# Optimization experiments

Measured on AMD Instinct MI355X. Metric: run time of the kernel, lower is better.

Reference implementation:

```python
import jax, jax.numpy as jnp
import numpy as np

DIM = 256; HEADS = 8; WS = 7; SHIFT = 3; HID = 1024
HD = DIM // HEADS
SCALE = HD ** -0.5
EPS = 1e-5


def layer_norm(x, g, b):
    m = x.mean(-1, keepdims=True)
    v = ((x - m) ** 2).mean(-1, keepdims=True)
    return (x - m) / jnp.sqrt(v + EPS) * g + b


def window_partition(x, ws):
    B, H, W, C = x.shape
    x = x.reshape(B, H // ws, ws, W // ws, ws, C).transpose(0, 1, 3, 2, 4, 5)
    return x.reshape(-1, ws * ws, C)


def window_reverse(w, ws, H, W):
    B = w.shape[0] // ((H // ws) * (W // ws))
    x = w.reshape(B, H // ws, W // ws, ws, ws, -1).transpose(0, 1, 3, 2, 4, 5)
    return x.reshape(B, H, W, -1)


def setup_inputs() -> dict:
    key = jax.random.key(0)
    ks = jax.random.split(key, 16)
    B, H, W, C = 4, 112, 112, DIM
    L = H * W; N = WS * WS; nW = (H // WS) * (W // WS)
    def p(k, shape, s=0.02):
        return jax.random.normal(k, shape, jnp.float32) * s
    return dict(
        x=jax.random.normal(ks[0], (B, L, C), jnp.float32),
        mask_matrix=jax.random.normal(ks[1], (nW, N, N), jnp.float32),
        polar_embed=jax.random.normal(ks[2], (B, L, 2), jnp.float32),
        vote_embed=jax.random.normal(ks[3], (B, L, 3), jnp.float32),
        g1=jnp.ones((C,), jnp.float32), be1=jnp.zeros((C,), jnp.float32),
        w_qkv=p(ks[4], (3 * C, C)), b_qkv=jnp.zeros((3 * C,), jnp.float32),
        w_proj=p(ks[5], (C, C)), b_proj=jnp.zeros((C,), jnp.float32),
        tau=jnp.ones((1, HEADS, 1, 1), jnp.float32),
        rpe_w1=p(ks[6], (16, 2)), rpe_b1=jnp.zeros((16,), jnp.float32),
        rpe_w2=p(ks[7], (HEADS, 16)), rpe_b2=jnp.zeros((HEADS,), jnp.float32),
        vote_w1=p(ks[8], (16, 3)), vote_b1=jnp.zeros((16,), jnp.float32),
        vote_w2=p(ks[9], (C, 16)), vote_b2=jnp.zeros((C,), jnp.float32),
        g2=jnp.ones((C,), jnp.float32), be2=jnp.zeros((C,), jnp.float32),
        fc1_w=p(ks[10], (HID, C)), fc1_b=jnp.zeros((HID,), jnp.float32),
        fc2_w=p(ks[11], (C, HID)), fc2_b=jnp.zeros((C,), jnp.float32),
        H=H, W=W)


def reference(x, mask_matrix, polar_embed, vote_embed, g1, be1, w_qkv, b_qkv,
              w_proj, b_proj, tau, rpe_w1, rpe_b1, rpe_w2, rpe_b2,
              vote_w1, vote_b1, vote_w2, vote_b2, g2, be2,
              fc1_w, fc1_b, fc2_w, fc2_b, H, W):
    B, L, C = x.shape
    shortcut = x
    xn = layer_norm(x, g1, be1).reshape(B, H, W, C)
    pe = polar_embed.reshape(B, H, W, -1)
    ve = vote_embed.reshape(B, H, W, -1)
    pad_b = (-H) % WS; pad_r = (-W) % WS
    if pad_b or pad_r:
        xn = jnp.pad(xn, ((0, 0), (0, pad_b), (0, pad_r), (0, 0)))
        pe = jnp.pad(pe, ((0, 0), (0, pad_b), (0, pad_r), (0, 0)))
        ve = jnp.pad(ve, ((0, 0), (0, pad_b), (0, pad_r), (0, 0)))
    Hp, Wp = H + pad_b, W + pad_r
    if SHIFT > 0:
        xn = jnp.roll(xn, (-SHIFT, -SHIFT), axis=(1, 2))
        pe = jnp.roll(pe, (-SHIFT, -SHIFT), axis=(1, 2))
        ve = jnp.roll(ve, (-SHIFT, -SHIFT), axis=(1, 2))
    xw = window_partition(xn, WS)   # [B_, N, C]
    pw = window_partition(pe, WS)   # [B_, N, 2]
    vw = window_partition(ve, WS)   # [B_, N, 3]
    B_, N, _ = xw.shape
    # vote mlp: 1x1 convs == pointwise linears over channel dim
    vlin = jax.nn.relu(vw @ vote_w1.T + vote_b1) @ vote_w2.T + vote_b2  # [B_, N, DIM]
    vemb = vlin.reshape(B_, N, HEADS, HD).transpose(0, 2, 1, 3)         # [B_, h, N, d]
    qkv = (xw @ w_qkv.T + b_qkv).reshape(B_, N, 3, HEADS, HD).transpose(2, 0, 3, 1, 4)
    q = qkv[0] + vemb; k = qkv[1] + vemb; v = qkv[2] + vemb
    qn = jnp.linalg.norm(q, axis=-1, keepdims=True)
    kn = jnp.linalg.norm(k, axis=-1, keepdims=True)
    attn = jnp.einsum('bhnd,bhmd->bhnm', q, k) * SCALE
    attn = attn / jnp.maximum(qn * kn.transpose(0, 1, 3, 2), 1e-6)
    attn = attn / jnp.clip(tau, 0.01, None)
    # relative pos bias: pairwise diff of polar embed through 1x1-conv MLP
    pT = pw.transpose(0, 2, 1)                  # [B_, 2, N]
    diff = pT[:, :, :, None] - pT[:, :, None, :]  # [B_, 2, N, N]
    r = jax.nn.relu(jnp.einsum('bcnm,oc->bonm', diff, rpe_w1) + rpe_b1[None, :, None, None])
    rpe = jnp.einsum('bonm,ho->bhnm', r, rpe_w2) + rpe_b2[None, :, None, None]
    attn = attn + rpe
    if SHIFT > 0:
        nW = mask_matrix.shape[0]
        attn = attn.reshape(B_ // nW, nW, HEADS, N, N) + mask_matrix[None, :, None]
        attn = attn.reshape(B_, HEADS, N, N)
    attn = jax.nn.softmax(attn, axis=-1)
    out = jnp.einsum('bhnm,bhmd->bhnd', attn, v + vemb)
    out = out.transpose(0, 2, 1, 3).reshape(B_, N, C) @ w_proj.T + b_proj
    xr = window_reverse(out, WS, Hp, Wp)
    if SHIFT > 0:
        xr = jnp.roll(xr, (SHIFT, SHIFT), axis=(1, 2))
    xr = xr[:, :H, :W, :].reshape(B, L, C)
    x = shortcut + xr
    y = layer_norm(x, g2, be2)
    y = jax.nn.gelu(y @ fc1_w.T + fc1_b, approximate=False) @ fc2_w.T + fc2_b
    return x + y
```

## Files before the change

### kernel.cpp

```cpp
#include <hip/hip_runtime.h>
#include <hip/hip_bf16.h>
#include <math.h>

using bf16 = __hip_bfloat16;
typedef __attribute__((ext_vector_type(8))) short short8;
typedef __attribute__((ext_vector_type(4))) float f32x4;
typedef unsigned int u32;

constexpr int BB    = 4;
constexpr int Hh    = 112;
constexpr int Ww    = 112;
constexpr int C     = 256;
constexpr int L     = Hh * Ww;
constexpr int HEADS = 8;
constexpr int WS    = 7;
constexpr int SHIFT = 3;
constexpr int HID   = 1024;
constexpr int HD    = 32;
constexpr int NWIN  = 49;
constexpr int NW    = 256;
constexpr int BT    = BB * NW;
constexpr int M     = BT * NWIN;
constexpr float SCALE = 0.17677669529663687f;
constexpr float EPS   = 1e-5f;

__device__ __forceinline__ int src_row_idx(int r) {
    int b_ = r / NWIN;
    int n  = r - b_ * NWIN;
    int b  = b_ >> 8;
    int w  = b_ & 255;
    int wh = w >> 4, ww = w & 15;
    int i  = n / WS, j = n - i * WS;
    int hp = wh * WS + i, wp = ww * WS + j;
    int h  = hp + SHIFT; if (h >= Hh) h -= Hh;
    int wc = wp + SHIFT; if (wc >= Ww) wc -= Ww;
    return b * L + h * Ww + wc;
}

__device__ __forceinline__ float bf2f(short s) {
    u32 u = ((u32)(unsigned short)s) << 16;
    float f; __builtin_memcpy(&f, &u, 4); return f;
}
__device__ __forceinline__ short f2bfbits(float f) {
    bf16 b = __float2bfloat16(f);
    short s; __builtin_memcpy(&s, &b, 2); return s;
}
__device__ __forceinline__ u32 pack2bf(float lo, float hi) {
    return (u32)(unsigned short)f2bfbits(lo) | ((u32)(unsigned short)f2bfbits(hi) << 16);
}

#define GL2LDS(g, l) __builtin_amdgcn_global_load_lds( \
    (const __attribute__((address_space(1))) u32*)(const void*)(g), \
    (__attribute__((address_space(3))) u32*)(void*)(l), 16, 0, 0)

__global__ __launch_bounds__(256)
void stats_kernel(const float* __restrict__ x, float* __restrict__ stats) {
    int wave = threadIdx.x >> 6, lane = threadIdx.x & 63;
    int tok  = blockIdx.x * 4 + wave;
    const float4 v = *(const float4*)&x[(size_t)tok * C + lane * 4];
    float s  = v.x + v.y + v.z + v.w;
    float s2 = v.x*v.x + v.y*v.y + v.z*v.z + v.w*v.w;
    #pragma unroll
    for (int o = 32; o > 0; o >>= 1) {
        s  += __shfl_down(s, o);
        s2 += __shfl_down(s2, o);
    }
    if (lane == 0) {
        float m   = s * (1.0f / C);
        float var = s2 * (1.0f / C) - m * m;
        stats[tok * 2]     = m;
        stats[tok * 2 + 1] = rsqrtf(var + EPS);
    }
}

__global__ __launch_bounds__(256)
void cvt_w(const float* __restrict__ in, bf16* __restrict__ o, int n4) {
    int i = blockIdx.x * 256 + threadIdx.x;
    if (i >= n4) return;
    float4 v = *(const float4*)&in[(size_t)i * 4];
    bf16 t4[4] = {__float2bfloat16(v.x), __float2bfloat16(v.y),
                  __float2bfloat16(v.z), __float2bfloat16(v.w)};
    *(uint2*)&o[(size_t)i * 4] = *(const uint2*)t4;
}

__global__ __launch_bounds__(256)
void vemb_kernel(const float* __restrict__ vote,
                 const float* __restrict__ w1, const float* __restrict__ b1,
                 const float* __restrict__ w2, const float* __restrict__ b2,
                 bf16* __restrict__ vemb) {
    __shared__ float w2s[256][16];
    __shared__ float b2s[256];
    __shared__ float w1s[48], b1s[16];
    const int tid = threadIdx.x;
    {
        const float4* src = (const float4*)(w2 + tid * 16);
        float4* dst = (float4*)&w2s[tid][0];
        dst[0] = src[0]; dst[1] = src[1]; dst[2] = src[2]; dst[3] = src[3];
        b2s[tid] = b2[tid];
        if (tid < 48) w1s[tid] = w1[tid];
        else if (tid < 64) b1s[tid - 48] = b1[tid - 48];
    }
    __syncthreads();

    const int r = blockIdx.x * 256 + tid;
    const int srow = src_row_idx(r);
    const float v0 = vote[(size_t)srow * 3];
    const float v1 = vote[(size_t)srow * 3 + 1];
    const float v2 = vote[(size_t)srow * 3 + 2];
    float hid[16];
    #pragma unroll
    for (int o = 0; o < 16; ++o)
        hid[o] = fmaxf(fmaf(w1s[o*3], v0, fmaf(w1s[o*3+1], v1, fmaf(w1s[o*3+2], v2, b1s[o]))), 0.f);

    bf16* orow = vemb + (size_t)r * 256;
    for (int c0 = 0; c0 < 256; c0 += 8) {
        bf16 t8[8];
        #pragma unroll
        for (int j = 0; j < 8; ++j) {
            const int c = c0 + j;
            float a = b2s[c];
            #pragma unroll
            for (int o = 0; o < 16; ++o) a = fmaf(hid[o], w2s[c][o], a);
            t8[j] = __float2bfloat16(a);
        }
        *(uint4*)&orow[c0] = *(const uint4*)t8;
    }
}

enum { MODE_QKV = 0, MODE_PROJ = 1, MODE_FC1 = 2, MODE_FC2 = 3 };

template <int MODE, int NT>
__global__ __launch_bounds__(256)
void mfma_gemm(const void* __restrict__ Asrc_, const bf16* __restrict__ Wb,
               const float* __restrict__ bias, const float* __restrict__ stats,
               const float* __restrict__ gamma, const float* __restrict__ beta,
               const bf16* __restrict__ vemb, const float* __restrict__ resid,
               void* __restrict__ outp) {
    constexpr int  K  = (MODE == MODE_FC2) ? 1024 : 256;
    constexpr bool LN = (MODE == MODE_QKV) || (MODE == MODE_FC1);
    __shared__ __align__(16) char lds[32768];
    char* ldsA = lds;
    char* ldsB = lds + 16384;

    const int tid  = threadIdx.x;
    const int lane = tid & 63;
    const int wid  = tid >> 6;
    const int wr   = wid >> 1, wc = wid & 1;
    const int lrow = lane & 15, lk = lane >> 4;

    const int cpx = gridDim.x >> 3;
    const int lg  = (blockIdx.x & 7) * cpx + (blockIdx.x >> 3);
    const int bx  = lg / NT, by = lg % NT;
    const int mBase = bx * 128, nBase = by * 128;

    const int s_sub = tid >> 3;
    const int chunk = tid & 7;
    const int s_dst = (chunk * 16) ^ ((s_sub & 7) << 4);
    const char* bSrc = (const char*)(Wb + (size_t)(nBase + s_sub) * K) + s_dst;
    const char* aSrcD = (const char*)((const bf16*)Asrc_ + (size_t)(mBase + s_sub) * K) + s_dst;

    int arow[4]; float amean[4], arstd[4];
    if constexpr (LN) {
        #pragma unroll
        for (int r = 0; r < 4; ++r) {
            int row  = mBase + r * 32 + s_sub;
            int srow = (MODE == MODE_QKV) ? src_row_idx(row) : row;
            arow[r] = srow;
            amean[r] = stats[srow * 2];
            arstd[r] = stats[srow * 2 + 1];
        }
    }

    f32x4 acc[4][4] = {};

    for (int t = 0; t < K / 64; ++t) {
        const int k0 = t * 64;
        if (t) __syncthreads();
        #pragma unroll
        for (int r = 0; r < 4; ++r)
            GL2LDS(bSrc + (size_t)r * 64 * K + (size_t)t * 128,
                   ldsB + r * 4096 + wid * 1024);
        if constexpr (!LN) {
            #pragma unroll
            for (int r = 0; r < 4; ++r)
                GL2LDS(aSrcD + (size_t)r * 64 * K + (size_t)t * 128,
                       ldsA + r * 4096 + wid * 1024);
        } else {
            const int kk = k0 + chunk * 8;
            float4 g0  = *(const float4*)&gamma[kk];
            float4 g1v = *(const float4*)&gamma[kk + 4];
            float4 b0  = *(const float4*)&beta[kk];
            float4 b1v = *(const float4*)&beta[kk + 4];
            #pragma unroll
            for (int r = 0; r < 4; ++r) {
                const float* src = (const float*)Asrc_ + (size_t)arow[r] * K + kk;
                float4 v0 = *(const float4*)src;
                float4 v1 = *(const float4*)(src + 4);
                float m = amean[r], sd = arstd[r];
                bf16 tb[8];
                tb[0] = __float2bfloat16((v0.x - m) * sd * g0.x  + b0.x);
                tb[1] = __float2bfloat16((v0.y - m) * sd * g0.y  + b0.y);
                tb[2] = __float2bfloat16((v0.z - m) * sd * g0.z  + b0.z);
                tb[3] = __float2bfloat16((v0.w - m) * sd * g0.w  + b0.w);
                tb[4] = __float2bfloat16((v1.x - m) * sd * g1v.x + b1v.x);
                tb[5] = __float2bfloat16((v1.y - m) * sd * g1v.y + b1v.y);
                tb[6] = __float2bfloat16((v1.z - m) * sd * g1v.z + b1v.z);
                tb[7] = __float2bfloat16((v1.w - m) * sd * g1v.w + b1v.w);
                *(short8*)(ldsA + (r * 32 + s_sub) * 128 + s_dst) = *(const short8*)tb;
            }
        }
        __syncthreads();
        const int sw = (lrow & 7) << 4;
        #pragma unroll
        for (int ks = 0; ks < 2; ++ks) {
            const int kbl = (ks * 64 + lk * 16) ^ sw;
            short8 af[4], bfr[4];
            #pragma unroll
            for (int q = 0; q < 4; ++q) {
                af[q]  = *(const short8*)(ldsA + (wr * 64 + q * 16 + lrow) * 128 + kbl);
                bfr[q] = *(const short8*)(ldsB + (wc * 64 + q * 16 + lrow) * 128 + kbl);
            }
            #pragma unroll
            for (int mi = 0; mi < 4; ++mi)
                #pragma unroll
                for (int ni = 0; ni < 4; ++ni)
                    acc[mi][ni] = __builtin_amdgcn_mfma_f32_16x16x32_bf16(
                        af[mi], bfr[ni], acc[mi][ni], 0, 0, 0);
        }
    }

    const int cB = nBase + wc * 64 + lrow;
    const int rB = mBase + wr * 64 + lk * 4;
    float bs[4];
    #pragma unroll
    for (int ni = 0; ni < 4; ++ni) bs[ni] = bias[cB + ni * 16];
    #pragma unroll
    for (int mi = 0; mi < 4; ++mi) {
        #pragma unroll
        for (int i = 0; i < 4; ++i) {
            const int r = rB + mi * 16 + i;
            const int dst = (MODE == MODE_PROJ) ? src_row_idx(r) : r;
            #pragma unroll
            for (int ni = 0; ni < 4; ++ni) {
                const int c = cB + ni * 16;
                float v = acc[mi][ni][i] + bs[ni];
                if constexpr (MODE == MODE_QKV) {
                    float ve = __bfloat162float(vemb[(size_t)r * 256 + (c & 255)]);
                    v += (c >= 512) ? 2.f * ve : ve;
                    ((bf16*)outp)[(size_t)r * 768 + c] = __float2bfloat16(v);
                } else if constexpr (MODE == MODE_PROJ) {
                    ((float*)outp)[(size_t)dst * 256 + c] =
                        resid[(size_t)dst * 256 + c] + v;
                } else if constexpr (MODE == MODE_FC1) {
                    float gl = 0.5f * v * (1.f + erff(v * 0.70710678118f));
                    ((bf16*)outp)[(size_t)r * 1024 + c] = __float2bfloat16(gl);
                } else {
                    ((float*)outp)[(size_t)r * 256 + c] =
                        resid[(size_t)r * 256 + c] + v;
                }
            }
        }
    }
}

__global__ __launch_bounds__(256)
void attn_kernel(const bf16* __restrict__ qkv, const float* __restrict__ polar,
                 const float* __restrict__ rw1, const float* __restrict__ rb1,
                 const float* __restrict__ rw2, const float* __restrict__ rb2,
                 const float* __restrict__ tau, const float* __restrict__ mask,
                 bf16* __restrict__ outp) {
    const int w  = blockIdx.x;
    const int wl = w & 255;
    const int t  = threadIdx.x;
    const int lane = t & 63, wid = t >> 6;
    const int l15 = lane & 15, q4 = lane >> 4;
    const size_t wbase = (size_t)w * NWIN;
    const short* qs = (const short*)qkv;

    __shared__ float pwx[NWIN], pwy[NWIN];
    __shared__ float rqn[8][64], rkn[8][64];
    __shared__ float cw1s[32], cb1s[16], cw2s[8][16], rb2s[8], scts[8];
    __shared__ short rpem[8][2401];

    if (t < 98) {
        int n = t >> 1, cix = t & 1;
        int srow = src_row_idx(w * NWIN + n);
        float v = polar[(size_t)srow * 2 + cix];
        if (cix) pwy[n] = v; else pwx[n] = v;
    }
    if (t >= 128 && t < 256) {
        int u = t - 128;
        if (u < 128) cw2s[u >> 4][u & 15] = rw2[u];
    }
    if (t < 32) cw1s[t] = rw1[t];
    else if (t < 48) cb1s[t - 32] = rb1[t - 32];
    else if (t < 56) rb2s[t - 48] = rb2[t - 48];
    else if (t < 64) scts[t - 56] = SCALE / fmaxf(tau[t - 56], 0.01f);

    for (int idx = t; idx < 8 * NWIN; idx += 256) {
        int h = idx / NWIN, n = idx - h * NWIN;
        const bf16* qp = qkv + (wbase + n) * 768 + h * 32;
        float sq = 0, sk = 0;
        #pragma unroll
        for (int c = 0; c < 4; ++c) {
            short8 qv = *(const short8*)(qp + c * 8);
            short8 kv = *(const short8*)(qp + 256 + c * 8);
            #pragma unroll
            for (int j = 0; j < 8; ++j) {
                float qf = bf2f(qv[j]); sq += qf * qf;
                float kf = bf2f(kv[j]); sk += kf * kf;
            }
        }
        rqn[h][n] = rsqrtf(sq);
        rkn[h][n] = rsqrtf(sk);
    }
    __syncthreads();

    for (int e = t; e < NWIN * NWIN; e += 256) {
        int n = e / NWIN, m = e - n * NWIN;
        float dx = pwx[n] - pwx[m], dy = pwy[n] - pwy[m];
        float hid[16];
        #pragma unroll
        for (int o = 0; o < 16; ++o)
            hid[o] = fmaxf(fmaf(cw1s[2*o], dx, fmaf(cw1s[2*o+1], dy, cb1s[o])), 0.f);
        float mv = mask[(size_t)wl * NWIN * NWIN + e];
        #pragma unroll
        for (int h = 0; h < 8; ++h) {
            float a = rb2s[h] + mv;
            #pragma unroll
            for (int o = 0; o < 16; ++o) a = fmaf(hid[o], cw2s[h][o], a);
            rpem[h][e] = f2bfbits(a);
        }
    }
    __syncthreads();

    const short8 z8 = {0,0,0,0,0,0,0,0};
    const int qa  = (q4 & 1) * 2;
    const int sel = q4 >> 1;

    for (int hh = 0; hh < 2; ++hh) {
        const int h = wid + hh * 4;
        const bf16* hbase = qkv + wbase * 768 + h * 32;
        const float sct = scts[h];

        short8 kf[4], qf[4];
        #pragma unroll
        for (int at = 0; at < 4; ++at) {
            int m = at * 16 + l15;
            kf[at] = (m < NWIN) ? *(const short8*)(hbase + (size_t)m * 768 + 256 + q4 * 8) : z8;
        }
        #pragma unroll
        for (int nt = 0; nt < 4; ++nt) {
            int n = nt * 16 + l15;
            qf[nt] = (n < NWIN) ? *(const short8*)(hbase + (size_t)n * 768 + q4 * 8) : z8;
        }
        short8 vb[2][2];
        #pragma unroll
        for (int ks = 0; ks < 2; ++ks)
            #pragma unroll
            for (int ct = 0; ct < 2; ++ct) {
                short tmp[8];
                #pragma unroll
                for (int j = 0; j < 8; ++j) {
                    int m = ks * 32 + q4 * 8 + j;
                    tmp[j] = (m < NWIN)
                        ? qs[(wbase + m) * 768 + 512 + h * 32 + ct * 16 + l15]
                        : (short)0;
                }
                __builtin_memcpy(&vb[ks][ct], tmp, 16);
            }

        u32 pw[4][4][2];
        const f32x4 zf = {0.f, 0.f, 0.f, 0.f};
        #pragma unroll
        for (int nt = 0; nt < 4; ++nt) {
            f32x4 sacc[4];
            #pragma unroll
            for (int at = 0; at < 4; ++at)
                sacc[at] = __builtin_amdgcn_mfma_f32_16x16x32_bf16(kf[at], qf[nt], zf, 0, 0, 0);
            const int n = nt * 16 + l15;
            const float rq = rqn[h][n];
            float pv[4][4];
            #pragma unroll
            for (int at = 0; at < 4; ++at)
                #pragma unroll
                for (int i = 0; i < 4; ++i) {
                    int m = at * 16 + q4 * 4 + i;
                    float val = -1e30f;
                    if (n < NWIN && m < NWIN) {
                        float rr = fminf(rq * rkn[h][m], 1e6f);
                        val = sacc[at][i] * sct * rr + bf2f(rpem[h][n * NWIN + m]);
                    }
                    pv[at][i] = val;
                }
            float mx = -1e30f;
            #pragma unroll
            for (int at = 0; at < 4; ++at)
                #pragma unroll
                for (int i = 0; i < 4; ++i) mx = fmaxf(mx, pv[at][i]);
            mx = fmaxf(mx, __shfl_xor(mx, 16));
            mx = fmaxf(mx, __shfl_xor(mx, 32));
            float sum = 0.f;
            #pragma unroll
            for (int at = 0; at < 4; ++at)
                #pragma unroll
                for (int i = 0; i < 4; ++i) {
                    float ev = __expf(pv[at][i] - mx);
                    pv[at][i] = ev; sum += ev;
                }
            sum += __shfl_xor(sum, 16);
            sum += __shfl_xor(sum, 32);
            const float inv = 1.0f / sum;
            #pragma unroll
            for (int at = 0; at < 4; ++at) {
                pw[nt][at][0] = pack2bf(pv[at][0] * inv, pv[at][1] * inv);
                pw[nt][at][1] = pack2bf(pv[at][2] * inv, pv[at][3] * inv);
            }
        }

        f32x4 o[4][2] = {};
        #pragma unroll
        for (int nt = 0; nt < 4; ++nt) {
            #pragma unroll
            for (int ks = 0; ks < 2; ++ks) {
                u32 wv[4];
                #pragma unroll
                for (int w_ = 0; w_ < 4; ++w_) {
                    int srcl = l15 + (qa + (w_ >> 1)) * 16;
                    u32 lo = (u32)__shfl((int)pw[nt][2 * ks][w_ & 1], srcl);
                    u32 hi = (u32)__shfl((int)pw[nt][2 * ks + 1][w_ & 1], srcl);
                    wv[w_] = sel ? hi : lo;
                }
                short8 pa;
                __builtin_memcpy(&pa, wv, 16);
                #pragma unroll
                for (int ct = 0; ct < 2; ++ct)
                    o[nt][ct] = __builtin_amdgcn_mfma_f32_16x16x32_bf16(pa, vb[ks][ct], o[nt][ct], 0, 0, 0);
            }
        }

        #pragma unroll
        for (int nt = 0; nt < 4; ++nt)
            #pragma unroll
            for (int ct = 0; ct < 2; ++ct)
                #pragma unroll
                for (int i = 0; i < 4; ++i) {
                    int n = nt * 16 + q4 * 4 + i;
                    if (n < NWIN)
                        outp[(wbase + n) * 256 + h * 32 + ct * 16 + l15] =
                            __float2bfloat16(o[nt][ct][i]);
                }
    }
}

extern "C" void kernel_launch(void* const* d_in, const int* in_sizes, int n_in,
                              void* d_out, int out_size, void* d_ws, size_t ws_size,
                              hipStream_t stream) {
    const float* x     = (const float*)d_in[0];
    const float* mask  = (const float*)d_in[1];
    const float* polar = (const float*)d_in[2];
    const float* vote  = (const float*)d_in[3];
    const float* g1    = (const float*)d_in[4];
    const float* be1   = (const float*)d_in[5];
    const float* wqkv  = (const float*)d_in[6];
    const float* bqkv  = (const float*)d_in[7];
    const float* wproj = (const float*)d_in[8];
    const float* bproj = (const float*)d_in[9];
    const float* tau   = (const float*)d_in[10];
    const float* rw1   = (const float*)d_in[11];
    const float* rb1   = (const float*)d_in[12];
    const float* rw2   = (const float*)d_in[13];
    const float* rb2   = (const float*)d_in[14];
    const float* vw1   = (const float*)d_in[15];
    const float* vb1   = (const float*)d_in[16];
    const float* vw2   = (const float*)d_in[17];
    const float* vb2   = (const float*)d_in[18];
    const float* g2    = (const float*)d_in[19];
    const float* be2   = (const float*)d_in[20];
    const float* fc1w  = (const float*)d_in[21];
    const float* fc1b  = (const float*)d_in[22];
    const float* fc2w  = (const float*)d_in[23];
    const float* fc2b  = (const float*)d_in[24];
    float* out = (float*)d_out;

    char* base = (char*)d_ws;
    bf16*  qkv     = (bf16*)base;
    bf16*  vemb    = (bf16*)(base + 77070336);
    bf16*  attnout = (bf16*)(base + 77070336);
    bf16*  hbuf    = (bf16*)base;
    bf16*  wqkvb   = (bf16*)(base + 102760448);
    bf16*  wprojb  = wqkvb + 768 * 256;
    bf16*  fc1wb   = wprojb + 256 * 256;
    bf16*  fc2wb   = fc1wb + 1024 * 256;
    float* stats1  = (float*)(base + 104333312);
    float* stats2  = stats1 + 2 * M;

    cvt_w<<<192, 256, 0, stream>>>(wqkv, wqkvb, 768*256/4);
    cvt_w<<<64,  256, 0, stream>>>(wproj, wprojb, 256*256/4);
    cvt_w<<<256, 256, 0, stream>>>(fc1w, fc1wb, 1024*256/4);
    cvt_w<<<256, 256, 0, stream>>>(fc2w, fc2wb, 256*1024/4);

    stats_kernel<<<M / 4, 256, 0, stream>>>(x, stats1);
    vemb_kernel<<<M / 256, 256, 0, stream>>>(vote, vw1, vb1, vw2, vb2, vemb);

    mfma_gemm<MODE_QKV, 6><<<(M / 128) * 6, 256, 0, stream>>>(
        x, wqkvb, bqkv, stats1, g1, be1, vemb, nullptr, qkv);

    attn_kernel<<<BT, 256, 0, stream>>>(qkv, polar, rw1, rb1, rw2, rb2, tau, mask, attnout);

    mfma_gemm<MODE_PROJ, 2><<<(M / 128) * 2, 256, 0, stream>>>(
        attnout, wprojb, bproj, nullptr, nullptr, nullptr, nullptr, x, out);

    stats_kernel<<<M / 4, 256, 0, stream>>>(out, stats2);

    mfma_gemm<MODE_FC1, 8><<<(M / 128) * 8, 256, 0, stream>>>(
        out, fc1wb, fc1b, stats2, g2, be2, nullptr, nullptr, hbuf);

    mfma_gemm<MODE_FC2, 2><<<(M / 128) * 2, 256, 0, stream>>>(
        hbuf, fc2wb, fc2b, nullptr, nullptr, nullptr, nullptr, out, out);
}
```

Baseline: 369.6 us.

## Double-buffer LDS tiles in MFMA GEMM to overlap loads with compute

Splits the shared-memory staging buffers into two halves and prefetches the next K-tile of A and B (global-to-LDS for B and non-LN A, register staging for LayerNorm A) while MFMAs run on the current tile. This halves the barriers per iteration and is meant to hide global-memory latency behind compute. LDS use doubles to 64 KB per block, which may reduce occupancy, and register pressure rises from the staged A values.

Measured after the change: 372.3 us. About the same (+0.7%).

```diff
diff --git a/kernel.cpp b/kernel.cpp
--- a/kernel.cpp
+++ b/kernel.cpp
@@ -137,10 +137,10 @@
                const bf16* __restrict__ vemb, const float* __restrict__ resid,
                void* __restrict__ outp) {
     constexpr int  K  = (MODE == MODE_FC2) ? 1024 : 256;
+    constexpr int  T  = K / 64;
     constexpr bool LN = (MODE == MODE_QKV) || (MODE == MODE_FC1);
-    __shared__ __align__(16) char lds[32768];
-    char* ldsA = lds;
-    char* ldsB = lds + 16384;
+    __shared__ __align__(16) char ldsA[2][16384];
+    __shared__ __align__(16) char ldsB[2][16384];
 
     const int tid  = threadIdx.x;
     const int lane = tid & 63;
@@ -156,7 +156,7 @@
     const int s_sub = tid >> 3;
     const int chunk = tid & 7;
     const int s_dst = (chunk * 16) ^ ((s_sub & 7) << 4);
-    const char* bSrc = (const char*)(Wb + (size_t)(nBase + s_sub) * K) + s_dst;
+    const char* bSrc  = (const char*)(Wb + (size_t)(nBase + s_sub) * K) + s_dst;
     const char* aSrcD = (const char*)((const bf16*)Asrc_ + (size_t)(mBase + s_sub) * K) + s_dst;
 
     int arow[4]; float amean[4], arstd[4];
@@ -171,54 +171,82 @@
         }
     }
 
+    float4 sa0[4], sa1[4];
+    float4 sg0, sg1, sb0, sb1;
+
+    auto issueA = [&](int tt) {
+        const int kk = tt * 64 + chunk * 8;
+        sg0 = *(const float4*)&gamma[kk];
+        sg1 = *(const float4*)&gamma[kk + 4];
+        sb0 = *(const float4*)&beta[kk];
+        sb1 = *(const float4*)&beta[kk + 4];
+        #pragma unroll
+        for (int r = 0; r < 4; ++r) {
+            const float* src = (const float*)Asrc_ + (size_t)arow[r] * K + kk;
+            sa0[r] = *(const float4*)src;
+            sa1[r] = *(const float4*)(src + 4);
+        }
+    };
+    auto writeA = [&](int tt) {
+        char* dst = ldsA[tt & 1];
+        #pragma unroll
+        for (int r = 0; r < 4; ++r) {
+            float m = amean[r], sd = arstd[r];
+            bf16 tb[8];
+            tb[0] = __float2bfloat16((sa0[r].x - m) * sd * sg0.x + sb0.x);
+            tb[1] = __float2bfloat16((sa0[r].y - m) * sd * sg0.y + sb0.y);
+            tb[2] = __float2bfloat16((sa0[r].z - m) * sd * sg0.z + sb0.z);
+            tb[3] = __float2bfloat16((sa0[r].w - m) * sd * sg0.w + sb0.w);
+            tb[4] = __float2bfloat16((sa1[r].x - m) * sd * sg1.x + sb1.x);
+            tb[5] = __float2bfloat16((sa1[r].y - m) * sd * sg1.y + sb1.y);
+            tb[6] = __float2bfloat16((sa1[r].z - m) * sd * sg1.z + sb1.z);
+            tb[7] = __float2bfloat16((sa1[r].w - m) * sd * sg1.w + sb1.w);
+            *(short8*)(dst + (r * 32 + s_sub) * 128 + s_dst) = *(const short8*)tb;
+        }
+    };
+
     f32x4 acc[4][4] = {};
-
-    for (int t = 0; t < K / 64; ++t) {
-        const int k0 = t * 64;
-        if (t) __syncthreads();
+    const int sw = (lrow & 7) << 4;
+
+    #pragma unroll
+    for (int r = 0; r < 4; ++r)
+        GL2LDS(bSrc + (size_t)r * 64 * K, ldsB[0] + r * 4096 + wid * 1024);
+    if constexpr (!LN) {
         #pragma unroll
         for (int r = 0; r < 4; ++r)
-            GL2LDS(bSrc + (size_t)r * 64 * K + (size_t)t * 128,
-                   ldsB + r * 4096 + wid * 1024);
-        if constexpr (!LN) {
+            GL2LDS(aSrcD + (size_t)r * 64 * K, ldsA[0] + r * 4096 + wid * 1024);
+    } else {
+        issueA(0);
+        writeA(0);
+    }
+    __syncthreads();
+
+    #pragma unroll
+    for (int t = 0; t < T; ++t) {
+        if (t + 1 < T) {
             #pragma unroll
             for (int r = 0; r < 4; ++r)
-                GL2LDS(aSrcD + (size_t)r * 64 * K + (size_t)t * 128,
-                       ldsA + r * 4096 + wid * 1024);
-        } else {
-            const int kk = k0 + chunk * 8;
-            float4 g0  = *(const float4*)&gamma[kk];
-            float4 g1v = *(const float4*)&gamma[kk + 4];
-            float4 b0  = *(const float4*)&beta[kk];
-            float4 b1v = *(const float4*)&beta[kk + 4];
-            #pragma unroll
-            for (int r = 0; r < 4; ++r) {
-                const float* src = (const float*)Asrc_ + (size_t)arow[r] * K + kk;
-                float4 v0 = *(const float4*)src;
-                float4 v1 = *(const float4*)(src + 4);
-                float m = amean[r], sd = arstd[r];
-                bf16 tb[8];
-                tb[0] = __float2bfloat16((v0.x - m) * sd * g0.x  + b0.x);
-                tb[1] = __float2bfloat16((v0.y - m) * sd * g0.y  + b0.y);
-                tb[2] = __float2bfloat16((v0.z - m) * sd * g0.z  + b0.z);
-                tb[3] = __float2bfloat16((v0.w - m) * sd * g0.w  + b0.w);
-                tb[4] = __float2bfloat16((v1.x - m) * sd * g1v.x + b1v.x);
-                tb[5] = __float2bfloat16((v1.y - m) * sd * g1v.y + b1v.y);
-                tb[6] = __float2bfloat16((v1.z - m) * sd * g1v.z + b1v.z);
-                tb[7] = __float2bfloat16((v1.w - m) * sd * g1v.w + b1v.w);
-                *(short8*)(ldsA + (r * 32 + s_sub) * 128 + s_dst) = *(const short8*)tb;
-            }
-        }
-        __syncthreads();
-        const int sw = (lrow & 7) << 4;
+                GL2LDS(bSrc + (size_t)r * 64 * K + (size_t)(t + 1) * 128,
+                       ldsB[(t + 1) & 1] + r * 4096 + wid * 1024);
+            if constexpr (!LN) {
+                #pragma unroll
+                for (int r = 0; r < 4; ++r)
+                    GL2LDS(aSrcD + (size_t)r * 64 * K + (size_t)(t + 1) * 128,
+                           ldsA[(t + 1) & 1] + r * 4096 + wid * 1024);
+            } else {
+                issueA(t + 1);
+            }
+        }
+        const char* cA = ldsA[t & 1];
+        const char* cB = ldsB[t & 1];
         #pragma unroll
         for (int ks = 0; ks < 2; ++ks) {
             const int kbl = (ks * 64 + lk * 16) ^ sw;
             short8 af[4], bfr[4];
             #pragma unroll
             for (int q = 0; q < 4; ++q) {
-                af[q]  = *(const short8*)(ldsA + (wr * 64 + q * 16 + lrow) * 128 + kbl);
-                bfr[q] = *(const short8*)(ldsB + (wc * 64 + q * 16 + lrow) * 128 + kbl);
+                af[q]  = *(const short8*)(cA + (wr * 64 + q * 16 + lrow) * 128 + kbl);
+                bfr[q] = *(const short8*)(cB + (wc * 64 + q * 16 + lrow) * 128 + kbl);
             }
             #pragma unroll
             for (int mi = 0; mi < 4; ++mi)
@@ -227,13 +255,17 @@
                     acc[mi][ni] = __builtin_amdgcn_mfma_f32_16x16x32_bf16(
                         af[mi], bfr[ni], acc[mi][ni], 0, 0, 0);
         }
-    }
-
-    const int cB = nBase + wc * 64 + lrow;
-    const int rB = mBase + wr * 64 + lk * 4;
+        if (t + 1 < T) {
+            if constexpr (LN) writeA(t + 1);
+            __syncthreads();
+        }
+    }
+
+    const int cBc = nBase + wc * 64 + lrow;
+    const int rB  = mBase + wr * 64 + lk * 4;
     float bs[4];
     #pragma unroll
-    for (int ni = 0; ni < 4; ++ni) bs[ni] = bias[cB + ni * 16];
+    for (int ni = 0; ni < 4; ++ni) bs[ni] = bias[cBc + ni * 16];
     #pragma unroll
     for (int mi = 0; mi < 4; ++mi) {
         #pragma unroll
@@ -242,7 +274,7 @@
             const int dst = (MODE == MODE_PROJ) ? src_row_idx(r) : r;
             #pragma unroll
             for (int ni = 0; ni < 4; ++ni) {
-                const int c = cB + ni * 16;
+                const int c = cBc + ni * 16;
                 float v = acc[mi][ni][i] + bs[ni];
                 if constexpr (MODE == MODE_QKV) {
                     float ve = __bfloat162float(vemb[(size_t)r * 256 + (c & 255)]);
```

## Fuse FC1, GELU and FC2 into one MLP kernel keeping hidden tile in LDS

Applied to the files above, without the earlier changes.

Replaces the separate FC1 and FC2 GEMMs with a single fused kernel. Each 64-row block computes the hidden activations chunk by chunk, applies GELU, stages them in LDS as bf16, and accumulates the FC2 output, so the large hidden buffer never round-trips through global memory. A new prep kernel applies LayerNorm2 and writes a bf16 normalized input in place of the stats pass. In exchange, the 64-row tiles give less weight reuse, the activation operand is read directly from global memory, and the loop has many barriers. Occupancy may also be lower because of the larger LDS footprint.

Measured after the change: 476.4 us. 1.29x slower.

```diff
diff --git a/kernel.cpp b/kernel.cpp
--- a/kernel.cpp
+++ b/kernel.cpp
@@ -74,6 +74,29 @@
 }
 
 __global__ __launch_bounds__(256)
+void prep2_kernel(const float* __restrict__ x, const float* __restrict__ g,
+                  const float* __restrict__ b, bf16* __restrict__ o) {
+    int wave = threadIdx.x >> 6, lane = threadIdx.x & 63;
+    int tok  = blockIdx.x * 4 + wave;
+    float4 v = *(const float4*)&x[(size_t)tok * C + lane * 4];
+    float s  = v.x + v.y + v.z + v.w;
+    float s2 = v.x*v.x + v.y*v.y + v.z*v.z + v.w*v.w;
+    #pragma unroll
+    for (int ofs = 32; ofs > 0; ofs >>= 1) {
+        s  += __shfl_xor(s, ofs);
+        s2 += __shfl_xor(s2, ofs);
+    }
+    float m    = s * (1.f / C);
+    float rstd = rsqrtf(s2 * (1.f / C) - m * m + EPS);
+    float4 gv = *(const float4*)&g[lane * 4];
+    float4 bv = *(const float4*)&b[lane * 4];
+    uint2 u;
+    u.x = pack2bf((v.x - m) * rstd * gv.x + bv.x, (v.y - m) * rstd * gv.y + bv.y);
+    u.y = pack2bf((v.z - m) * rstd * gv.z + bv.z, (v.w - m) * rstd * gv.w + bv.w);
+    *(uint2*)&o[(size_t)tok * C + lane * 4] = u;
+}
+
+__global__ __launch_bounds__(256)
 void cvt_w(const float* __restrict__ in, bf16* __restrict__ o, int n4) {
     int i = blockIdx.x * 256 + threadIdx.x;
     if (i >= n4) return;
@@ -127,7 +150,7 @@
     }
 }
 
-enum { MODE_QKV = 0, MODE_PROJ = 1, MODE_FC1 = 2, MODE_FC2 = 3 };
+enum { MODE_QKV = 0, MODE_PROJ = 1 };
 
 template <int MODE, int NT>
 __global__ __launch_bounds__(256)
@@ -136,8 +159,8 @@
                const float* __restrict__ gamma, const float* __restrict__ beta,
                const bf16* __restrict__ vemb, const float* __restrict__ resid,
                void* __restrict__ outp) {
-    constexpr int  K  = (MODE == MODE_FC2) ? 1024 : 256;
-    constexpr bool LN = (MODE == MODE_QKV) || (MODE == MODE_FC1);
+    constexpr int  K  = 256;
+    constexpr bool LN = (MODE == MODE_QKV);
     __shared__ __align__(16) char lds[32768];
     char* ldsA = lds;
     char* ldsB = lds + 16384;
@@ -164,7 +187,7 @@
         #pragma unroll
         for (int r = 0; r < 4; ++r) {
             int row  = mBase + r * 32 + s_sub;
-            int srow = (MODE == MODE_QKV) ? src_row_idx(row) : row;
+            int srow = src_row_idx(row);
             arow[r] = srow;
             amean[r] = stats[srow * 2];
             arstd[r] = stats[srow * 2 + 1];
@@ -248,19 +271,126 @@
                     float ve = __bfloat162float(vemb[(size_t)r * 256 + (c & 255)]);
                     v += (c >= 512) ? 2.f * ve : ve;
                     ((bf16*)outp)[(size_t)r * 768 + c] = __float2bfloat16(v);
-                } else if constexpr (MODE == MODE_PROJ) {
+                } else {
                     ((float*)outp)[(size_t)dst * 256 + c] =
                         resid[(size_t)dst * 256 + c] + v;
-                } else if constexpr (MODE == MODE_FC1) {
-                    float gl = 0.5f * v * (1.f + erff(v * 0.70710678118f));
-                    ((bf16*)outp)[(size_t)r * 1024 + c] = __float2bfloat16(gl);
-                } else {
-                    ((float*)outp)[(size_t)r * 256 + c] =
-                        resid[(size_t)r * 256 + c] + v;
                 }
             }
         }
     }
+}
+
+__global__ __launch_bounds__(256)
+void fused_mlp(const bf16* __restrict__ x2n, const bf16* __restrict__ w1b,
+               const float* __restrict__ fb1, const bf16* __restrict__ w2b,
+               const float* __restrict__ fb2, float* __restrict__ outp) {
+    __shared__ __align__(16) char ldsH[16384];
+    __shared__ __align__(16) char ldsBU[32768];
+
+    const int tid  = threadIdx.x;
+    const int lane = tid & 63, wid = tid >> 6;
+    const int lrow = lane & 15, lk = lane >> 4;
+    const int mBase = blockIdx.x * 64;
+    const int s_sub = tid >> 3;
+    const int chunk = tid & 7;
+    const int s_dst = (chunk * 16) ^ ((s_sub & 7) << 4);
+    const int sw = (lrow & 7) << 4;
+
+    f32x4 acc2[4][4] = {};
+
+    for (int hc = 0; hc < 8; ++hc) {
+        f32x4 acc1[2][4] = {};
+        for (int t = 0; t < 4; ++t) {
+            #pragma unroll
+            for (int r = 0; r < 4; ++r)
+                GL2LDS((const char*)w1b + (size_t)(hc * 128 + r * 32 + s_sub) * 512
+                           + t * 128 + s_dst,
+                       ldsBU + r * 4096 + wid * 1024);
+            short8 bA[4][2];
+            #pragma unroll
+            for (int ni = 0; ni < 4; ++ni)
+                #pragma unroll
+                for (int ks = 0; ks < 2; ++ks)
+                    bA[ni][ks] = *(const short8*)(x2n
+                        + (size_t)(mBase + ni * 16 + lrow) * 256
+                        + t * 64 + ks * 32 + lk * 8);
+            __syncthreads();
+            #pragma unroll
+            for (int ks = 0; ks < 2; ++ks) {
+                const int kbl = (ks * 64 + lk * 16) ^ sw;
+                short8 af[2];
+                af[0] = *(const short8*)(ldsBU + (wid * 32 + lrow) * 128 + kbl);
+                af[1] = *(const short8*)(ldsBU + (wid * 32 + 16 + lrow) * 128 + kbl);
+                #pragma unroll
+                for (int mi = 0; mi < 2; ++mi)
+                    #pragma unroll
+                    for (int ni = 0; ni < 4; ++ni)
+                        acc1[mi][ni] = __builtin_amdgcn_mfma_f32_16x16x32_bf16(
+                            af[mi], bA[ni][ks], acc1[mi][ni], 0, 0, 0);
+            }
+            __syncthreads();
+        }
+        #pragma unroll
+        for (int mi = 0; mi < 2; ++mi) {
+            const int hidb = wid * 32 + mi * 16 + lk * 4;
+            float4 fb = *(const float4*)&fb1[hc * 128 + hidb];
+            float fbv[4] = {fb.x, fb.y, fb.z, fb.w};
+            #pragma unroll
+            for (int ni = 0; ni < 4; ++ni) {
+                const int r = ni * 16 + lrow;
+                float gg[4];
+                #pragma unroll
+                for (int i = 0; i < 4; ++i) {
+                    float v = acc1[mi][ni][i] + fbv[i];
+                    gg[i] = 0.5f * v * (1.f + erff(v * 0.70710678118f));
+                }
+                uint2 u;
+                u.x = pack2bf(gg[0], gg[1]);
+                u.y = pack2bf(gg[2], gg[3]);
+                *(uint2*)(ldsH + r * 256 + ((hidb * 2) ^ ((r & 7) << 4))) = u;
+            }
+        }
+        __syncthreads();
+        #pragma unroll
+        for (int s2 = 0; s2 < 2; ++s2) {
+            #pragma unroll
+            for (int r = 0; r < 8; ++r)
+                GL2LDS((const char*)w2b + (size_t)(r * 32 + s_sub) * 2048
+                           + hc * 256 + s2 * 128 + s_dst,
+                       ldsBU + r * 4096 + wid * 1024);
+            __syncthreads();
+            #pragma unroll
+            for (int ks = 0; ks < 2; ++ks) {
+                const int kbl = (ks * 64 + lk * 16) ^ sw;
+                short8 ah[4], bw[4];
+                #pragma unroll
+                for (int mi = 0; mi < 4; ++mi)
+                    ah[mi] = *(const short8*)(ldsH + (mi * 16 + lrow) * 256
+                        + ((s2 * 128 + ks * 64 + lk * 16) ^ sw));
+                #pragma unroll
+                for (int ni = 0; ni < 4; ++ni)
+                    bw[ni] = *(const short8*)(ldsBU + (wid * 64 + ni * 16 + lrow) * 128 + kbl);
+                #pragma unroll
+                for (int mi = 0; mi < 4; ++mi)
+                    #pragma unroll
+                    for (int ni = 0; ni < 4; ++ni)
+                        acc2[mi][ni] = __builtin_amdgcn_mfma_f32_16x16x32_bf16(
+                            ah[mi], bw[ni], acc2[mi][ni], 0, 0, 0);
+            }
+            __syncthreads();
+        }
+    }
+    #pragma unroll
+    for (int mi = 0; mi < 4; ++mi)
+        #pragma unroll
+        for (int i = 0; i < 4; ++i) {
+            const int r = mBase + mi * 16 + lk * 4 + i;
+            #pragma unroll
+            for (int ni = 0; ni < 4; ++ni) {
+                const int oc = wid * 64 + ni * 16 + lrow;
+                outp[(size_t)r * 256 + oc] += acc2[mi][ni][i] + fb2[oc];
+            }
+        }
 }
 
 __global__ __launch_bounds__(256)
@@ -487,13 +617,12 @@
     bf16*  qkv     = (bf16*)base;
     bf16*  vemb    = (bf16*)(base + 77070336);
     bf16*  attnout = (bf16*)(base + 77070336);
-    bf16*  hbuf    = (bf16*)base;
+    bf16*  x2n     = (bf16*)(base + 77070336);
     bf16*  wqkvb   = (bf16*)(base + 102760448);
     bf16*  wprojb  = wqkvb + 768 * 256;
     bf16*  fc1wb   = wprojb + 256 * 256;
     bf16*  fc2wb   = fc1wb + 1024 * 256;
     float* stats1  = (float*)(base + 104333312);
-    float* stats2  = stats1 + 2 * M;
 
     cvt_w<<<192, 256, 0, stream>>>(wqkv, wqkvb, 768*256/4);
     cvt_w<<<64,  256, 0, stream>>>(wproj, wprojb, 256*256/4);
@@ -511,11 +640,7 @@
     mfma_gemm<MODE_PROJ, 2><<<(M / 128) * 2, 256, 0, stream>>>(
         attnout, wprojb, bproj, nullptr, nullptr, nullptr, nullptr, x, out);
 
-    stats_kernel<<<M / 4, 256, 0, stream>>>(out, stats2);
-
-    mfma_gemm<MODE_FC1, 8><<<(M / 128) * 8, 256, 0, stream>>>(
-        out, fc1wb, fc1b, stats2, g2, be2, nullptr, nullptr, hbuf);
-
-    mfma_gemm<MODE_FC2, 2><<<(M / 128) * 2, 256, 0, stream>>>(
-        hbuf, fc2wb, fc2b, nullptr, nullptr, nullptr, nullptr, out, out);
-}
+    prep2_kernel<<<M / 4, 256, 0, stream>>>(out, g2, be2, x2n);
+
+    fused_mlp<<<M / 64, 256, 0, stream>>>(x2n, fc1wb, fc1b, fc2wb, fc2b, out);
+}
```

## Materialize LayerNorm output as bf16 before GEMMs instead of fusing into A-load

Applied to the files above, without the earlier changes.

The stats kernel becomes a full LayerNorm kernel that gathers shifted/windowed rows, normalizes, applies gamma/beta and writes a bf16 buffer. The QKV and FC1 GEMMs then load A through the async global-to-LDS path instead of reading fp32 rows and normalizing in registers on every N-tile. This removes redundant fp32 reads and normalization repeated across 6 or 8 column tiles. In exchange it adds an extra bf16 write and read of a full activation buffer.

Result: no change. 366.8 us (-0.7%).

```diff
diff --git a/kernel.cpp b/kernel.cpp
--- a/kernel.cpp
+++ b/kernel.cpp
@@ -54,23 +54,27 @@
     (__attribute__((address_space(3))) u32*)(void*)(l), 16, 0, 0)
 
 __global__ __launch_bounds__(256)
-void stats_kernel(const float* __restrict__ x, float* __restrict__ stats) {
+void prep_ln(const float* __restrict__ x, const float* __restrict__ g,
+             const float* __restrict__ b, bf16* __restrict__ o, int gather) {
     int wave = threadIdx.x >> 6, lane = threadIdx.x & 63;
-    int tok  = blockIdx.x * 4 + wave;
-    const float4 v = *(const float4*)&x[(size_t)tok * C + lane * 4];
+    int tok = blockIdx.x * 4 + wave;
+    int srow = gather ? src_row_idx(tok) : tok;
+    float4 v = *(const float4*)&x[(size_t)srow * C + lane * 4];
     float s  = v.x + v.y + v.z + v.w;
     float s2 = v.x*v.x + v.y*v.y + v.z*v.z + v.w*v.w;
     #pragma unroll
-    for (int o = 32; o > 0; o >>= 1) {
-        s  += __shfl_down(s, o);
-        s2 += __shfl_down(s2, o);
-    }
-    if (lane == 0) {
-        float m   = s * (1.0f / C);
-        float var = s2 * (1.0f / C) - m * m;
-        stats[tok * 2]     = m;
-        stats[tok * 2 + 1] = rsqrtf(var + EPS);
-    }
+    for (int ofs = 32; ofs > 0; ofs >>= 1) {
+        s  += __shfl_xor(s, ofs);
+        s2 += __shfl_xor(s2, ofs);
+    }
+    float m    = s * (1.f / C);
+    float rstd = rsqrtf(s2 * (1.f / C) - m * m + EPS);
+    float4 gv = *(const float4*)&g[lane * 4];
+    float4 bv = *(const float4*)&b[lane * 4];
+    uint2 u;
+    u.x = pack2bf((v.x - m) * rstd * gv.x + bv.x, (v.y - m) * rstd * gv.y + bv.y);
+    u.y = pack2bf((v.z - m) * rstd * gv.z + bv.z, (v.w - m) * rstd * gv.w + bv.w);
+    *(uint2*)&o[(size_t)tok * C + lane * 4] = u;
 }
 
 __global__ __launch_bounds__(256)
@@ -131,13 +135,11 @@
 
 template <int MODE, int NT>
 __global__ __launch_bounds__(256)
-void mfma_gemm(const void* __restrict__ Asrc_, const bf16* __restrict__ Wb,
-               const float* __restrict__ bias, const float* __restrict__ stats,
-               const float* __restrict__ gamma, const float* __restrict__ beta,
+void mfma_gemm(const bf16* __restrict__ A, const bf16* __restrict__ Wb,
+               const float* __restrict__ bias,
                const bf16* __restrict__ vemb, const float* __restrict__ resid,
                void* __restrict__ outp) {
-    constexpr int  K  = (MODE == MODE_FC2) ? 1024 : 256;
-    constexpr bool LN = (MODE == MODE_QKV) || (MODE == MODE_FC1);
+    constexpr int K = (MODE == MODE_FC2) ? 1024 : 256;
     __shared__ __align__(16) char lds[32768];
     char* ldsA = lds;
     char* ldsB = lds + 16384;
@@ -157,57 +159,18 @@
     const int chunk = tid & 7;
     const int s_dst = (chunk * 16) ^ ((s_sub & 7) << 4);
     const char* bSrc = (const char*)(Wb + (size_t)(nBase + s_sub) * K) + s_dst;
-    const char* aSrcD = (const char*)((const bf16*)Asrc_ + (size_t)(mBase + s_sub) * K) + s_dst;
-
-    int arow[4]; float amean[4], arstd[4];
-    if constexpr (LN) {
+    const char* aSrc = (const char*)(A  + (size_t)(mBase + s_sub) * K) + s_dst;
+
+    f32x4 acc[4][4] = {};
+
+    for (int t = 0; t < K / 64; ++t) {
+        if (t) __syncthreads();
         #pragma unroll
         for (int r = 0; r < 4; ++r) {
-            int row  = mBase + r * 32 + s_sub;
-            int srow = (MODE == MODE_QKV) ? src_row_idx(row) : row;
-            arow[r] = srow;
-            amean[r] = stats[srow * 2];
-            arstd[r] = stats[srow * 2 + 1];
-        }
-    }
-
-    f32x4 acc[4][4] = {};
-
-    for (int t = 0; t < K / 64; ++t) {
-        const int k0 = t * 64;
-        if (t) __syncthreads();
-        #pragma unroll
-        for (int r = 0; r < 4; ++r)
             GL2LDS(bSrc + (size_t)r * 64 * K + (size_t)t * 128,
                    ldsB + r * 4096 + wid * 1024);
-        if constexpr (!LN) {
-            #pragma unroll
-            for (int r = 0; r < 4; ++r)
-                GL2LDS(aSrcD + (size_t)r * 64 * K + (size_t)t * 128,
-                       ldsA + r * 4096 + wid * 1024);
-        } else {
-            const int kk = k0 + chunk * 8;
-            float4 g0  = *(const float4*)&gamma[kk];
-            float4 g1v = *(const float4*)&gamma[kk + 4];
-            float4 b0  = *(const float4*)&beta[kk];
-            float4 b1v = *(const float4*)&beta[kk + 4];
-            #pragma unroll
-            for (int r = 0; r < 4; ++r) {
-                const float* src = (const float*)Asrc_ + (size_t)arow[r] * K + kk;
-                float4 v0 = *(const float4*)src;
-                float4 v1 = *(const float4*)(src + 4);
-                float m = amean[r], sd = arstd[r];
-                bf16 tb[8];
-                tb[0] = __float2bfloat16((v0.x - m) * sd * g0.x  + b0.x);
-                tb[1] = __float2bfloat16((v0.y - m) * sd * g0.y  + b0.y);
-                tb[2] = __float2bfloat16((v0.z - m) * sd * g0.z  + b0.z);
-                tb[3] = __float2bfloat16((v0.w - m) * sd * g0.w  + b0.w);
-                tb[4] = __float2bfloat16((v1.x - m) * sd * g1v.x + b1v.x);
-                tb[5] = __float2bfloat16((v1.y - m) * sd * g1v.y + b1v.y);
-                tb[6] = __float2bfloat16((v1.z - m) * sd * g1v.z + b1v.z);
-                tb[7] = __float2bfloat16((v1.w - m) * sd * g1v.w + b1v.w);
-                *(short8*)(ldsA + (r * 32 + s_sub) * 128 + s_dst) = *(const short8*)tb;
-            }
+            GL2LDS(aSrc + (size_t)r * 64 * K + (size_t)t * 128,
+                   ldsA + r * 4096 + wid * 1024);
         }
         __syncthreads();
         const int sw = (lrow & 7) << 4;
@@ -492,30 +455,29 @@
     bf16*  wprojb  = wqkvb + 768 * 256;
     bf16*  fc1wb   = wprojb + 256 * 256;
     bf16*  fc2wb   = fc1wb + 1024 * 256;
-    float* stats1  = (float*)(base + 104333312);
-    float* stats2  = stats1 + 2 * M;
+    bf16*  lnbuf   = (bf16*)(base + 105136128);
 
     cvt_w<<<192, 256, 0, stream>>>(wqkv, wqkvb, 768*256/4);
     cvt_w<<<64,  256, 0, stream>>>(wproj, wprojb, 256*256/4);
     cvt_w<<<256, 256, 0, stream>>>(fc1w, fc1wb, 1024*256/4);
     cvt_w<<<256, 256, 0, stream>>>(fc2w, fc2wb, 256*1024/4);
 
-    stats_kernel<<<M / 4, 256, 0, stream>>>(x, stats1);
+    prep_ln<<<M / 4, 256, 0, stream>>>(x, g1, be1, lnbuf, 1);
     vemb_kernel<<<M / 256, 256, 0, stream>>>(vote, vw1, vb1, vw2, vb2, vemb);
 
     mfma_gemm<MODE_QKV, 6><<<(M / 128) * 6, 256, 0, stream>>>(
-        x, wqkvb, bqkv, stats1, g1, be1, vemb, nullptr, qkv);
+        lnbuf, wqkvb, bqkv, vemb, nullptr, qkv);
 
     attn_kernel<<<BT, 256, 0, stream>>>(qkv, polar, rw1, rb1, rw2, rb2, tau, mask, attnout);
 
     mfma_gemm<MODE_PROJ, 2><<<(M / 128) * 2, 256, 0, stream>>>(
-        attnout, wprojb, bproj, nullptr, nullptr, nullptr, nullptr, x, out);
-
-    stats_kernel<<<M / 4, 256, 0, stream>>>(out, stats2);
+        attnout, wprojb, bproj, nullptr, x, out);
+
+    prep_ln<<<M / 4, 256, 0, stream>>>(out, g2, be2, lnbuf, 0);
 
     mfma_gemm<MODE_FC1, 8><<<(M / 128) * 8, 256, 0, stream>>>(
-        out, fc1wb, fc1b, stats2, g2, be2, nullptr, nullptr, hbuf);
+        lnbuf, fc1wb, fc1b, nullptr, nullptr, hbuf);
 
     mfma_gemm<MODE_FC2, 2><<<(M / 128) * 2, 256, 0, stream>>>(
-        hbuf, fc2wb, fc2b, nullptr, nullptr, nullptr, nullptr, out, out);
-}
+        hbuf, fc2wb, fc2b, nullptr, out, out);
+}
```
